# Optimization experiments

Hardware: AMD Instinct MI355X
Metric: run time of the kernel (lower is better)

Reference implementation:

```python
import jax, jax.numpy as jnp
import numpy as np

DIM = 512
HEADS = 8
DIM_HEAD = 64
SLICE = 32
INNER = HEADS * DIM_HEAD  # 512


def setup_inputs() -> dict:
    key = jax.random.key(0)
    ks = jax.random.split(key, 8)
    B, N = 8, 8192
    s = 0.02
    return {
        "x": jax.random.normal(ks[0], (B, N, DIM), dtype=jnp.float32),
        "W_in": jax.random.normal(ks[1], (DIM, INNER), dtype=jnp.float32) * s,
        "b_in": jnp.zeros((INNER,), dtype=jnp.float32),
        "Wq": jax.random.normal(ks[2], (DIM_HEAD, SLICE), dtype=jnp.float32) * s,
        "Wk": jax.random.normal(ks[3], (DIM_HEAD, SLICE), dtype=jnp.float32) * s,
        "Wv": jax.random.normal(ks[4], (DIM_HEAD, DIM_HEAD), dtype=jnp.float32) * s,
        "W_out": jax.random.normal(ks[5], (INNER, DIM), dtype=jnp.float32) * s,
        "b_out": jnp.zeros((DIM,), dtype=jnp.float32),
    }


def reference(x, W_in, b_in, Wq, Wk, Wv, W_out, b_out):
    B, N, C = x.shape
    # input projection -> [B, H, N, Dh]
    x_mid = (x @ W_in + b_in).reshape(B, N, HEADS, DIM_HEAD).transpose(0, 2, 1, 3)
    q = x_mid @ Wq            # [B,H,N,S]
    k = x_mid @ Wk            # [B,H,N,S]
    v = x_mid @ Wv            # [B,H,N,Dh]
    q = jax.nn.softmax(q, axis=-1)   # over slice dim
    k = jax.nn.softmax(k, axis=-2)   # over sequence dim
    kv = jnp.einsum('bhns,bhnc->bhsc', k, v)   # [B,H,S,Dh]
    qkv = jnp.einsum('bhns,bhsc->bhnc', q, kv)  # [B,H,N,Dh]
    qkv = qkv.transpose(0, 2, 1, 3).reshape(B, N, INNER)  # b n (h d)
    return qkv @ W_out + b_out
```

## Files before the change

kernel.cpp:

```cpp
#include <hip/hip_runtime.h>
#include <cstdint>
#include <cstddef>

typedef __bf16 bf16_t;
typedef __bf16 bf16x8 __attribute__((ext_vector_type(8)));
typedef __bf16 bf16x4 __attribute__((ext_vector_type(4)));
typedef float  f32x4  __attribute__((ext_vector_type(4)));

#define HEADS    8
#define DIM_HEAD 64
#define SLICE    32
#define DIMC     512
#define NCOL     1024
#define BATCH    8
#define NSEQ     8192
#define NTOK     65536

__device__ __forceinline__ void gl2lds16(const bf16_t* g, bf16_t* l) {
  __builtin_amdgcn_global_load_lds(
      (const __attribute__((address_space(1))) uint32_t*)g,
      (__attribute__((address_space(3))) uint32_t*)l, 16, 0, 0);
}

__global__ __launch_bounds__(256) void xcast_kernel(const float* __restrict__ x,
                                                    bf16_t* __restrict__ xb) {
  const size_t i = ((size_t)blockIdx.x * 256 + threadIdx.x) * 8;
  const float4 a = *reinterpret_cast<const float4*>(x + i);
  const float4 b = *reinterpret_cast<const float4*>(x + i + 4);
  bf16x8 w;
  w[0] = (bf16_t)a.x; w[1] = (bf16_t)a.y; w[2] = (bf16_t)a.z; w[3] = (bf16_t)a.w;
  w[4] = (bf16_t)b.x; w[5] = (bf16_t)b.y; w[6] = (bf16_t)b.z; w[7] = (bf16_t)b.w;
  *reinterpret_cast<bf16x8*>(xb + i) = w;
}

__global__ __launch_bounds__(256) void wprep_kernel(
    const float* __restrict__ W_in, const float* __restrict__ b_in,
    const float* __restrict__ Wq,   const float* __restrict__ Wk,
    const float* __restrict__ Wv,
    bf16_t* __restrict__ WcT, float* __restrict__ bias_c) {
  __shared__ float sW[8192];
  for (int t = threadIdx.x; t < 2048; t += 256) { sW[t] = Wq[t]; sW[2048 + t] = Wk[t]; }
  for (int t = threadIdx.x; t < 4096; t += 256) sW[4096 + t] = Wv[t];
  __syncthreads();

  const int T  = blockIdx.x * 256 + threadIdx.x;
  const int NT = gridDim.x * 256;
  for (int idx = T; idx < NCOL * DIMC; idx += NT) {
    const int col = idx >> 9, cin = idx & 511;
    int base, ldw, h, j;
    if (col < 256)      { h = col >> 5;       j = col & 31;       base = 0;    ldw = 32; }
    else if (col < 512) { h = (col-256) >> 5; j = (col-256) & 31; base = 2048; ldw = 32; }
    else                { h = (col-512) >> 6; j = (col-512) & 63; base = 4096; ldw = 64; }
    const float4* vp = reinterpret_cast<const float4*>(W_in + (size_t)cin * DIMC + h * DIM_HEAD);
    float acc = 0.f;
    #pragma unroll
    for (int d4 = 0; d4 < 16; ++d4) {
      const float4 v = vp[d4];
      acc += v.x * sW[base + (4*d4+0)*ldw + j];
      acc += v.y * sW[base + (4*d4+1)*ldw + j];
      acc += v.z * sW[base + (4*d4+2)*ldw + j];
      acc += v.w * sW[base + (4*d4+3)*ldw + j];
    }
    WcT[(size_t)col * DIMC + cin] = (bf16_t)acc;
  }
  if (T < NCOL) {
    const int col = T;
    int base, ldw, h, j;
    if (col < 256)      { h = col >> 5;       j = col & 31;       base = 0;    ldw = 32; }
    else if (col < 512) { h = (col-256) >> 5; j = (col-256) & 31; base = 2048; ldw = 32; }
    else                { h = (col-512) >> 6; j = (col-512) & 63; base = 4096; ldw = 64; }
    const float* vec = b_in + h * DIM_HEAD;
    float acc = 0.f;
    #pragma unroll 8
    for (int d = 0; d < DIM_HEAD; ++d) acc += vec[d] * sW[base + d * ldw + j];
    bias_c[col] = acc;
  }
}

template<int EPI>
__global__ __launch_bounds__(256) void gemm_kernel(
    const bf16_t* __restrict__ A, const bf16_t* __restrict__ Bt,
    void* __restrict__ Cv, const float* __restrict__ bias,
    int K, int lda, int ldc,
    size_t strideA, size_t strideB, size_t strideC)
{
  __shared__ bf16_t As[128 * 64];
  __shared__ bf16_t Bs[128 * 64];
  const int tid  = threadIdx.x;
  const int m0   = blockIdx.y * 128;
  const int n0   = blockIdx.x * 128;
  const int bz   = blockIdx.z;
  const int wave = tid >> 6, lane = tid & 63;
  const int cg   = lane & 15, qd = lane >> 4;
  const int wm   = (wave & 1) * 64, wn = (wave >> 1) * 64;
  const int srow   = lane >> 3;
  const int gchunk = (lane & 7) ^ srow;
  const int chb    = cg & 7;

  const bf16_t* Ab = A  + strideA * bz;
  const bf16_t* Bb = Bt + strideB * bz;

  f32x4 acc[4][4];
  #pragma unroll
  for (int i = 0; i < 4; ++i)
    #pragma unroll
    for (int j = 0; j < 4; ++j) acc[i][j] = (f32x4){0.f, 0.f, 0.f, 0.f};

  for (int k0 = 0; k0 < K; k0 += 64) {
    __syncthreads();
    #pragma unroll
    for (int i = 0; i < 4; ++i) {
      const int c = wave * 4 + i;
      const int row = c * 8 + srow;
      gl2lds16(Ab + (size_t)(m0 + row) * lda + k0 + gchunk * 8, As + c * 512 + lane * 8);
    }
    #pragma unroll
    for (int i = 0; i < 4; ++i) {
      const int c = wave * 4 + i;
      const int row = c * 8 + srow;
      gl2lds16(Bb + (size_t)(n0 + row) * K + k0 + gchunk * 8, Bs + c * 512 + lane * 8);
    }
    __syncthreads();
    #pragma unroll
    for (int ks = 0; ks < 64; ks += 32) {
      const int k4 = ks >> 3;
      bf16x8 af[4], bfr[4];
      #pragma unroll
      for (int i = 0; i < 4; ++i) {
        const int ch = (qd + k4) ^ chb;
        af[i] = *reinterpret_cast<const bf16x8*>(As + (wm + 16*i + cg) * 64 + ch * 8);
      }
      #pragma unroll
      for (int j = 0; j < 4; ++j) {
        const int ch = (qd + k4) ^ chb;
        bfr[j] = *reinterpret_cast<const bf16x8*>(Bs + (wn + 16*j + cg) * 64 + ch * 8);
      }
      #pragma unroll
      for (int i = 0; i < 4; ++i)
        #pragma unroll
        for (int j = 0; j < 4; ++j)
          acc[i][j] = __builtin_amdgcn_mfma_f32_16x16x32_bf16(af[i], bfr[j], acc[i][j], 0, 0, 0);
    }
  }

  #pragma unroll
  for (int j = 0; j < 4; ++j) {
    const int col = n0 + wn + 16 * j + cg;
    const float bv = bias[col];
    #pragma unroll
    for (int i = 0; i < 4; ++i) {
      #pragma unroll
      for (int rr = 0; rr < 4; ++rr) {
        const int row = m0 + wm + 16 * i + qd * 4 + rr;
        float v = acc[i][j][rr] + bv;
        if (EPI == 1) {
          if (col >= 256 && col < 512) v = __expf(v);
          ((bf16_t*)Cv + strideC * bz)[(size_t)row * ldc + col] = (bf16_t)v;
        } else {
          ((float*)Cv + strideC * bz)[(size_t)row * ldc + col] = v;
        }
      }
    }
  }
}

__global__ __launch_bounds__(256) void kv_accum_kernel(const bf16_t* __restrict__ qkv1,
                                                       float* __restrict__ kv_num,
                                                       float* __restrict__ kv_den) {
  const int chunk = blockIdx.x;
  const int h = blockIdx.y, b = blockIdx.z;
  const int tid = threadIdx.x;
  const int wave = tid >> 6, lane = tid & 63;
  const int cgrp = lane & 15, sgrp = lane >> 4;
  const int c0 = cgrp * 4, s0 = sgrp * 8;

  float acc[8][4];
  float dacc[8];
  #pragma unroll
  for (int i = 0; i < 8; ++i) {
    dacc[i] = 0.f;
    #pragma unroll
    for (int j = 0; j < 4; ++j) acc[i][j] = 0.f;
  }

  const int nbase = chunk * 512 + wave * 128;
  const bf16_t* base = qkv1 + ((size_t)(b * NSEQ + nbase)) * NCOL;
  const int ek_off = 256 + h * SLICE + s0;
  const int v_off  = 512 + h * DIM_HEAD + c0;

  #pragma unroll 4
  for (int n = 0; n < 128; ++n) {
    const bf16_t* rowp = base + (size_t)n * NCOL;
    bf16x8 ek = *reinterpret_cast<const bf16x8*>(rowp + ek_off);
    bf16x4 vv = *reinterpret_cast<const bf16x4*>(rowp + v_off);
    float ekf[8], vf[4];
    #pragma unroll
    for (int i = 0; i < 8; ++i) ekf[i] = (float)ek[i];
    #pragma unroll
    for (int j = 0; j < 4; ++j) vf[j] = (float)vv[j];
    #pragma unroll
    for (int i = 0; i < 8; ++i) {
      dacc[i] += ekf[i];
      #pragma unroll
      for (int j = 0; j < 4; ++j) acc[i][j] += ekf[i] * vf[j];
    }
  }

  __shared__ float red[4][SLICE][DIM_HEAD];
  __shared__ float redd[4][SLICE];
  #pragma unroll
  for (int i = 0; i < 8; ++i)
    #pragma unroll
    for (int j = 0; j < 4; ++j) red[wave][s0 + i][c0 + j] = acc[i][j];
  if (cgrp == 0) {
    #pragma unroll
    for (int i = 0; i < 8; ++i) redd[wave][s0 + i] = dacc[i];
  }
  __syncthreads();
  float* dstn = kv_num + (size_t)(b * HEADS + h) * (SLICE * DIM_HEAD);
  for (int t = tid; t < SLICE * DIM_HEAD; t += 256) {
    const int s = t >> 6, c = t & 63;
    atomicAdd(&dstn[t], red[0][s][c] + red[1][s][c] + red[2][s][c] + red[3][s][c]);
  }
  if (tid < SLICE)
    atomicAdd(&kv_den[(b * HEADS + h) * SLICE + tid],
              redd[0][tid] + redd[1][tid] + redd[2][tid] + redd[3][tid]);
}

__global__ __launch_bounds__(256) void softmax_q_kernel(bf16_t* __restrict__ qkv1) {
  const int T = blockIdx.x * 256 + threadIdx.x;
  const int token = T >> 3, h = T & 7;
  bf16_t* p = qkv1 + (size_t)token * NCOL + h * SLICE;
  bf16x8 d[4];
  #pragma unroll
  for (int i = 0; i < 4; ++i) d[i] = reinterpret_cast<const bf16x8*>(p)[i];
  float f[32];
  #pragma unroll
  for (int i = 0; i < 4; ++i)
    #pragma unroll
    for (int j = 0; j < 8; ++j) f[i * 8 + j] = (float)d[i][j];
  float m = f[0];
  #pragma unroll
  for (int i = 1; i < 32; ++i) m = fmaxf(m, f[i]);
  float s = 0.f;
  #pragma unroll
  for (int i = 0; i < 32; ++i) { f[i] = __expf(f[i] - m); s += f[i]; }
  const float rs = 1.f / s;
  #pragma unroll
  for (int i = 0; i < 4; ++i) {
    bf16x8 w;
    #pragma unroll
    for (int j = 0; j < 8; ++j) w[j] = (bf16_t)(f[i * 8 + j] * rs);
    reinterpret_cast<bf16x8*>(p)[i] = w;
  }
}

__global__ __launch_bounds__(512) void mprep_kernel(const float* __restrict__ kv_num,
                                                    const float* __restrict__ kv_den,
                                                    const float* __restrict__ W_out,
                                                    bf16_t* __restrict__ Mt) {
  const int bh = blockIdx.x, b = bh >> 3, h = bh & 7;
  const int tid = threadIdx.x;
  __shared__ float kvn[SLICE][DIM_HEAD];
  __shared__ float wbuf[8][DIMC];
  const float* src = kv_num + (size_t)bh * (SLICE * DIM_HEAD);
  for (int t = tid; t < SLICE * DIM_HEAD; t += 512)
    kvn[t >> 6][t & 63] = src[t] / kv_den[bh * SLICE + (t >> 6)];
  float accs[SLICE];
  #pragma unroll
  for (int s = 0; s < SLICE; ++s) accs[s] = 0.f;
  for (int cb = 0; cb < DIM_HEAD; cb += 8) {
    __syncthreads();
    for (int t = tid; t < 8 * DIMC; t += 512)
      wbuf[t >> 9][t & 511] = W_out[(size_t)(h * DIM_HEAD + cb + (t >> 9)) * DIMC + (t & 511)];
    __syncthreads();
    #pragma unroll
    for (int cc = 0; cc < 8; ++cc) {
      const float wv = wbuf[cc][tid];
      #pragma unroll
      for (int s = 0; s < SLICE; ++s) accs[s] += kvn[s][cb + cc] * wv;
    }
  }
  bf16_t* dst = Mt + (size_t)b * (DIMC * 256) + (size_t)tid * 256 + h * SLICE;
  #pragma unroll
  for (int s = 0; s < SLICE; ++s) dst[s] = (bf16_t)accs[s];
}

extern "C" void kernel_launch(void* const* d_in, const int* in_sizes, int n_in,
                              void* d_out, int out_size, void* d_ws, size_t ws_size,
                              hipStream_t stream) {
  const float* x     = (const float*)d_in[0];
  const float* W_in  = (const float*)d_in[1];
  const float* b_in  = (const float*)d_in[2];
  const float* Wq    = (const float*)d_in[3];
  const float* Wk    = (const float*)d_in[4];
  const float* Wv    = (const float*)d_in[5];
  const float* W_out = (const float*)d_in[6];
  const float* b_out = (const float*)d_in[7];
  float* out = (float*)d_out;

  uint8_t* ws = (uint8_t*)d_ws;
  bf16_t* qkv1   = (bf16_t*)(ws);
  bf16_t* WcT    = (bf16_t*)(ws + 134217728ull);
  float*  bias_c = (float*) (ws + 135266304ull);
  float*  kv_num = (float*) (ws + 135270400ull);
  float*  kv_den = (float*) (ws + 135794688ull);
  bf16_t* Mt     = (bf16_t*)(ws + 135802880ull);
  bf16_t* xb = (bf16_t*)d_out;

  hipMemsetAsync(kv_num, 0, 532480, stream);

  xcast_kernel<<<dim3(NTOK * DIMC / 8 / 256), dim3(256), 0, stream>>>(x, xb);
  wprep_kernel<<<dim3(256), dim3(256), 0, stream>>>(W_in, b_in, Wq, Wk, Wv, WcT, bias_c);

  gemm_kernel<1><<<dim3(8, 512, 1), dim3(256), 0, stream>>>(
      xb, WcT, (void*)qkv1, bias_c,
      512 , 512 , NCOL , (size_t)0, (size_t)0, (size_t)0);

  kv_accum_kernel<<<dim3(16, HEADS, BATCH), dim3(256), 0, stream>>>(qkv1, kv_num, kv_den);
  softmax_q_kernel<<<dim3(NTOK * HEADS / 256), dim3(256), 0, stream>>>(qkv1);
  mprep_kernel<<<dim3(BATCH * HEADS), dim3(512), 0, stream>>>(kv_num, kv_den, W_out, Mt);

  gemm_kernel<0><<<dim3(4, 64, BATCH), dim3(256), 0, stream>>>(
      qkv1, Mt, (void*)out, b_out,
      256 , NCOL , DIMC ,
      (size_t)NSEQ * NCOL, (size_t)DIMC * 256, (size_t)NSEQ * DIMC);
}
```

Before: 529.6 us.

## Fuse query slice softmax into projection GEMM epilogue and swizzle block order

The per-head softmax over the 32 query slice columns now runs inside the first GEMM's epilogue, using wave shuffles across the 16 column lanes. This removes the separate softmax_q kernel and its extra read and write pass over the query part of the intermediate buffer. Both GEMM instantiations also remap the linear block index so groups of 8 M-tiles are walked across all N-tiles, which is meant to improve L2 reuse of the A tiles. The cost is more shuffle and exp work in the epilogue, plus scalar bf16 stores for the query columns.

```diff
diff --git a/kernel.cpp b/kernel.cpp
--- a/kernel.cpp
+++ b/kernel.cpp
@@ -86,10 +86,14 @@
 {
   __shared__ bf16_t As[128 * 64];
   __shared__ bf16_t Bs[128 * 64];
-  const int tid  = threadIdx.x;
-  const int m0   = blockIdx.y * 128;
-  const int n0   = blockIdx.x * 128;
-  const int bz   = blockIdx.z;
+  const int tid = threadIdx.x;
+  const int p = blockIdx.y * gridDim.x + blockIdx.x;
+  int mblk, nblk;
+  if (EPI == 1) { mblk = (p & 7) + ((p >> 6) << 3); nblk = (p >> 3) & 7; }
+  else          { mblk = (p & 7) + ((p >> 5) << 3); nblk = (p >> 3) & 3; }
+  const int m0 = mblk * 128;
+  const int n0 = nblk * 128;
+  const int bz = blockIdx.z;
   const int wave = tid >> 6, lane = tid & 63;
   const int cg   = lane & 15, qd = lane >> 4;
   const int wm   = (wave & 1) * 64, wn = (wave >> 1) * 64;
@@ -143,21 +147,50 @@
     }
   }
 
-  #pragma unroll
-  for (int j = 0; j < 4; ++j) {
-    const int col = n0 + wn + 16 * j + cg;
-    const float bv = bias[col];
-    #pragma unroll
-    for (int i = 0; i < 4; ++i) {
-      #pragma unroll
-      for (int rr = 0; rr < 4; ++rr) {
-        const int row = m0 + wm + 16 * i + qd * 4 + rr;
-        float v = acc[i][j][rr] + bv;
-        if (EPI == 1) {
-          if (col >= 256 && col < 512) v = __expf(v);
-          ((bf16_t*)Cv + strideC * bz)[(size_t)row * ldc + col] = (bf16_t)v;
-        } else {
-          ((float*)Cv + strideC * bz)[(size_t)row * ldc + col] = v;
+  if (EPI == 1 && n0 < 256) {
+    #pragma unroll
+    for (int jp = 0; jp < 2; ++jp) {
+      const int j0 = 2 * jp, j1 = 2 * jp + 1;
+      const float b0 = bias[n0 + wn + 16 * j0 + cg];
+      const float b1 = bias[n0 + wn + 16 * j1 + cg];
+      #pragma unroll
+      for (int i = 0; i < 4; ++i) {
+        #pragma unroll
+        for (int rr = 0; rr < 4; ++rr) {
+          float v0 = acc[i][j0][rr] + b0;
+          float v1 = acc[i][j1][rr] + b1;
+          float mx = fmaxf(v0, v1);
+          #pragma unroll
+          for (int d = 1; d < 16; d <<= 1) mx = fmaxf(mx, __shfl_xor(mx, d, 64));
+          const float e0 = __expf(v0 - mx), e1 = __expf(v1 - mx);
+          float s = e0 + e1;
+          #pragma unroll
+          for (int d = 1; d < 16; d <<= 1) s += __shfl_xor(s, d, 64);
+          const float rs = 1.f / s;
+          const int row = m0 + wm + 16 * i + qd * 4 + rr;
+          bf16_t* crow = (bf16_t*)Cv + (size_t)row * ldc;
+          crow[n0 + wn + 16 * j0 + cg] = (bf16_t)(e0 * rs);
+          crow[n0 + wn + 16 * j1 + cg] = (bf16_t)(e1 * rs);
+        }
+      }
+    }
+  } else {
+    #pragma unroll
+    for (int j = 0; j < 4; ++j) {
+      const int col = n0 + wn + 16 * j + cg;
+      const float bv = bias[col];
+      #pragma unroll
+      for (int i = 0; i < 4; ++i) {
+        #pragma unroll
+        for (int rr = 0; rr < 4; ++rr) {
+          const int row = m0 + wm + 16 * i + qd * 4 + rr;
+          float v = acc[i][j][rr] + bv;
+          if (EPI == 1) {
+            if (col < 512) v = __expf(v);
+            ((bf16_t*)Cv + strideC * bz)[(size_t)row * ldc + col] = (bf16_t)v;
+          } else {
+            ((float*)Cv + strideC * bz)[(size_t)row * ldc + col] = v;
+          }
         }
       }
     }
@@ -225,34 +258,6 @@
   if (tid < SLICE)
     atomicAdd(&kv_den[(b * HEADS + h) * SLICE + tid],
               redd[0][tid] + redd[1][tid] + redd[2][tid] + redd[3][tid]);
-}
-
-__global__ __launch_bounds__(256) void softmax_q_kernel(bf16_t* __restrict__ qkv1) {
-  const int T = blockIdx.x * 256 + threadIdx.x;
-  const int token = T >> 3, h = T & 7;
-  bf16_t* p = qkv1 + (size_t)token * NCOL + h * SLICE;
-  bf16x8 d[4];
-  #pragma unroll
-  for (int i = 0; i < 4; ++i) d[i] = reinterpret_cast<const bf16x8*>(p)[i];
-  float f[32];
-  #pragma unroll
-  for (int i = 0; i < 4; ++i)
-    #pragma unroll
-    for (int j = 0; j < 8; ++j) f[i * 8 + j] = (float)d[i][j];
-  float m = f[0];
-  #pragma unroll
-  for (int i = 1; i < 32; ++i) m = fmaxf(m, f[i]);
-  float s = 0.f;
-  #pragma unroll
-  for (int i = 0; i < 32; ++i) { f[i] = __expf(f[i] - m); s += f[i]; }
-  const float rs = 1.f / s;
-  #pragma unroll
-  for (int i = 0; i < 4; ++i) {
-    bf16x8 w;
-    #pragma unroll
-    for (int j = 0; j < 8; ++j) w[j] = (bf16_t)(f[i * 8 + j] * rs);
-    reinterpret_cast<bf16x8*>(p)[i] = w;
-  }
 }
 
 __global__ __launch_bounds__(512) void mprep_kernel(const float* __restrict__ kv_num,
@@ -297,7 +302,6 @@
   const float* Wv    = (const float*)d_in[5];
   const float* W_out = (const float*)d_in[6];
   const float* b_out = (const float*)d_in[7];
-  float* out = (float*)d_out;
 
   uint8_t* ws = (uint8_t*)d_ws;
   bf16_t* qkv1   = (bf16_t*)(ws);
@@ -318,11 +322,10 @@
       512 , 512 , NCOL , (size_t)0, (size_t)0, (size_t)0);
 
   kv_accum_kernel<<<dim3(16, HEADS, BATCH), dim3(256), 0, stream>>>(qkv1, kv_num, kv_den);
-  softmax_q_kernel<<<dim3(NTOK * HEADS / 256), dim3(256), 0, stream>>>(qkv1);
   mprep_kernel<<<dim3(BATCH * HEADS), dim3(512), 0, stream>>>(kv_num, kv_den, W_out, Mt);
 
   gemm_kernel<0><<<dim3(4, 64, BATCH), dim3(256), 0, stream>>>(
-      qkv1, Mt, (void*)out, b_out,
+      qkv1, Mt, d_out, b_out,
       256 , NCOL , DIMC ,
       (size_t)NSEQ * NCOL, (size_t)DIMC * 256, (size_t)NSEQ * DIMC);
 }
```

Result: no change. 526.6 us (-0.6%).
